# Performance work log

Measured on AMD Instinct MI355X. Metric: run time of the kernel, lower is better.

Reference implementation:

```python
import jax, jax.numpy as jnp
import numpy as np

H = 128  # hidden_size
EPS = 1e-5


def _lstm_scan(pre, Whh, h0, c0):
    # pre: [L, B, 4H] = x @ Wih^T + bias, precomputed outside the scan
    def step(carry, g_in):
        h, c = carry
        gates = g_in + h @ Whh.T  # [B, 4H], PyTorch gate order i,f,g,o
        i, f, g, o = jnp.split(gates, 4, axis=-1)
        c = jax.nn.sigmoid(f) * c + jax.nn.sigmoid(i) * jnp.tanh(g)
        h = jax.nn.sigmoid(o) * jnp.tanh(c)
        return (h, c), h
    (_, _), hs = jax.lax.scan(step, (h0, c0), pre)
    return hs  # [L, B, H]


def setup_inputs() -> dict:
    key = jax.random.key(0)
    ks = jax.random.split(key, 12)
    B, L, D = 128, 512, 256
    s = 0.05
    inp = {
        "x": jax.random.normal(ks[0], (B, L, D), jnp.float32),
        "W_proj": jax.random.normal(ks[1], (D, D), jnp.float32) * s,
        "b_proj": jnp.zeros((D,), jnp.float32),
        "Wih_f": jax.random.normal(ks[2], (4 * H, D), jnp.float32) * s,
        "Whh_f": jax.random.normal(ks[3], (4 * H, H), jnp.float32) * s,
        "b_f": jnp.concatenate([jnp.zeros(H), jnp.ones(H), jnp.zeros(2 * H)]).astype(jnp.float32),
        "Wih_b": jax.random.normal(ks[4], (4 * H, D), jnp.float32) * s,
        "Whh_b": jax.random.normal(ks[5], (4 * H, H), jnp.float32) * s,
        "b_b": jnp.concatenate([jnp.zeros(H), jnp.ones(H), jnp.zeros(2 * H)]).astype(jnp.float32),
        "gamma": jnp.ones((2 * H,), jnp.float32),
        "beta": jnp.zeros((2 * H,), jnp.float32),
    }
    return inp


def reference(x, W_proj, b_proj, Wih_f, Whh_f, b_f, Wih_b, Whh_b, b_b, gamma, beta):
    B, L, D = x.shape
    # input projection
    xp = x @ W_proj.T + b_proj  # [B, L, D]
    xt = jnp.transpose(xp, (1, 0, 2))  # time-major [L, B, D]

    h0 = jnp.zeros((B, H), x.dtype)
    c0 = jnp.zeros((B, H), x.dtype)

    # precompute input contributions to gates (big batched GEMM)
    pre_f = jnp.einsum('lbd,gd->lbg', xt, Wih_f) + b_f  # [L, B, 4H]
    pre_b = jnp.einsum('lbd,gd->lbg', xt[::-1], Wih_b) + b_b

    hs_f = _lstm_scan(pre_f, Whh_f, h0, c0)           # [L, B, H]
    hs_b = _lstm_scan(pre_b, Whh_b, h0, c0)[::-1]     # reverse back to forward time

    out = jnp.concatenate([hs_f, hs_b], axis=-1)       # [L, B, 2H]
    out = jnp.transpose(out, (1, 0, 2))                # [B, L, 2H]

    # LayerNorm over last dim (eval mode; dropout is identity)
    mu = out.mean(axis=-1, keepdims=True)
    var = out.var(axis=-1, keepdims=True)
    out = (out - mu) * jax.lax.rsqrt(var + EPS) * gamma + beta
    return out
```

## Files before the change

### kernel.cpp

```cpp
#include <hip/hip_runtime.h>

#define NB 128
#define NL 512
#define ND 256
#define NG 1024

typedef __attribute__((ext_vector_type(8))) short bfv8;
typedef __attribute__((ext_vector_type(4))) float f32x4;

#define LOG2E 1.4426950408889634f
#define NSCALE (-1.4426950408889634f)
#define GSCALE (2.8853900817779268f)

__device__ __forceinline__ unsigned short f2bf(float f) {
    unsigned u = __float_as_uint(f);
    u += 0x7fffu + ((u >> 16) & 1u);
    return (unsigned short)(u >> 16);
}
__device__ __forceinline__ float bf2f(unsigned short u) {
    return __uint_as_float(((unsigned)u) << 16);
}

__global__ __launch_bounds__(256) void convert_kernel(const float* __restrict__ x,
                                                      unsigned short* __restrict__ xbt) {
    size_t t = (size_t)blockIdx.x * 256 + threadIdx.x;
    size_t e = t * 4;
    int d = (int)(e & 255u);
    int l = (int)((e >> 8) & 511u);
    int b = (int)(e >> 17);
    float4 v = *(const float4*)(x + e);
    ushort4 o;
    o.x = f2bf(v.x); o.y = f2bf(v.y); o.z = f2bf(v.z); o.w = f2bf(v.w);
    *(ushort4*)(xbt + ((size_t)(l * NB + b)) * ND + d) = o;
}

__global__ __launch_bounds__(256) void fold_kernel(const float* __restrict__ Wproj,
                                                   const float* __restrict__ bproj,
                                                   const float* __restrict__ Wih_f,
                                                   const float* __restrict__ b_f,
                                                   const float* __restrict__ Wih_b,
                                                   const float* __restrict__ b_b,
                                                   unsigned short* __restrict__ weff,
                                                   float* __restrict__ beff) {
    int g = blockIdx.x;
    int k = threadIdx.x;
    int dirg = g >> 9;
    int rem  = g & 511;
    int hidg = rem >> 2;
    int gate = rem & 3;
    int srcrow = gate * 128 + hidg;
    float scale = (gate == 2) ? GSCALE : NSCALE;
    const float* Wih = dirg ? (Wih_b + (size_t)srcrow * ND) : (Wih_f + (size_t)srcrow * ND);
    float acc = 0.f;
    for (int d = 0; d < ND; ++d)
        acc += Wih[d] * Wproj[(size_t)d * ND + k];
    weff[(size_t)g * ND + k] = f2bf(acc * scale);
    if (k == 0) {
        float ab = dirg ? b_b[srcrow] : b_f[srcrow];
        for (int d = 0; d < ND; ++d) ab += Wih[d] * bproj[d];
        beff[g] = ab * scale;
    }
}

__global__ __launch_bounds__(256, 2) void gemm_pre(const unsigned short* __restrict__ A,
                                                   const unsigned short* __restrict__ Bw,
                                                   const float* __restrict__ bias,
                                                   unsigned short* __restrict__ C) {
    __shared__ unsigned short As[128 * 32];
    __shared__ unsigned short Bs[128 * 32];
    const int tid = threadIdx.x;
    const int lane = tid & 63;
    const int wid = tid >> 6;
    const int m0 = blockIdx.y * 128;
    const int n0 = blockIdx.x * 128;
    const int wm = (wid >> 1) * 64;
    const int wn = (wid & 1) * 64;

    f32x4 acc[4][4] = {};

    const int row0 = tid >> 2;
    const int row1 = row0 + 64;
    const int co = (tid & 3) * 8;
    const int sw = (((tid & 3) << 4) ^ ((row0 & 3) << 4)) >> 1;

    bfv8 ra0 = *(const bfv8*)(A + (size_t)(m0 + row0) * ND + co);
    bfv8 ra1 = *(const bfv8*)(A + (size_t)(m0 + row1) * ND + co);
    bfv8 rb0 = *(const bfv8*)(Bw + (size_t)(n0 + row0) * ND + co);
    bfv8 rb1 = *(const bfv8*)(Bw + (size_t)(n0 + row1) * ND + co);

    for (int it = 0; it < 8; ++it) {
        __syncthreads();
        *(bfv8*)(As + row0 * 32 + sw) = ra0;
        *(bfv8*)(As + row1 * 32 + sw) = ra1;
        *(bfv8*)(Bs + row0 * 32 + sw) = rb0;
        *(bfv8*)(Bs + row1 * 32 + sw) = rb1;
        const int k1 = ((it + 1) & 7) * 32;
        ra0 = *(const bfv8*)(A + (size_t)(m0 + row0) * ND + k1 + co);
        ra1 = *(const bfv8*)(A + (size_t)(m0 + row1) * ND + k1 + co);
        rb0 = *(const bfv8*)(Bw + (size_t)(n0 + row0) * ND + k1 + co);
        rb1 = *(const bfv8*)(Bw + (size_t)(n0 + row1) * ND + k1 + co);
        __syncthreads();

        const int r = lane & 15;
        const int kq = lane >> 4;
        bfv8 af[4], bfr[4];
        #pragma unroll
        for (int m = 0; m < 4; ++m) {
            int rw = wm + m * 16 + r;
            af[m] = *(const bfv8*)(As + rw * 32 + (((kq << 4) ^ ((rw & 3) << 4)) >> 1));
        }
        #pragma unroll
        for (int n = 0; n < 4; ++n) {
            int rw = wn + n * 16 + r;
            bfr[n] = *(const bfv8*)(Bs + rw * 32 + (((kq << 4) ^ ((rw & 3) << 4)) >> 1));
        }
        #pragma unroll
        for (int m = 0; m < 4; ++m)
            #pragma unroll
            for (int n = 0; n < 4; ++n)
                acc[m][n] = __builtin_amdgcn_mfma_f32_16x16x32_bf16(af[m], bfr[n], acc[m][n], 0, 0, 0);
    }

    const int r = lane & 15;
    const int rq = lane >> 4;
    #pragma unroll
    for (int n = 0; n < 4; ++n) {
        int col = n0 + wn + n * 16 + r;
        float bv = bias[col];
        #pragma unroll
        for (int m = 0; m < 4; ++m) {
            #pragma unroll
            for (int v = 0; v < 4; ++v) {
                int rowg = m0 + wm + m * 16 + rq * 4 + v;
                C[(size_t)rowg * NG + col] = f2bf(acc[m][n][v] + bv);
            }
        }
    }
}

struct ScanSM {
    unsigned short h[2][136];
    char pin[81700];
};

#define MFMA16(a, b, c) __builtin_amdgcn_mfma_f32_16x16x32_bf16((a), (b), (c), 0, 0, 0)

#define STEP(S, CURB, NXTB)                                                    \
  {                                                                            \
    int rr = (S) + 2; if (rr > 511) rr = 511;                \
    int tts = dirs ? (511 - rr) : rr;                                          \
    const unsigned short* rowp = pdb + (size_t)tts * (NB * NG);                \
    uint2 nx = *(const uint2*)(rowp + hid4);                \
    bfv8 ha0 = *(const bfv8*)&sm.h[CURB][q * 8];                               \
    bfv8 ha1 = *(const bfv8*)&sm.h[CURB][32 + q * 8];                          \
    bfv8 ha2 = *(const bfv8*)&sm.h[CURB][64 + q * 8];                          \
    bfv8 ha3 = *(const bfv8*)&sm.h[CURB][96 + q * 8];                          \
    f32x4 z = {0.f, 0.f, 0.f, 0.f};                                            \
    f32x4 acci = MFMA16(ha0, bfr[0][0], z);                                    \
    f32x4 accf = MFMA16(ha0, bfr[1][0], z);                                    \
    f32x4 accg = MFMA16(ha0, bfr[2][0], z);                                    \
    f32x4 acco = MFMA16(ha0, bfr[3][0], z);                                    \
    acci = MFMA16(ha1, bfr[0][1], acci); accf = MFMA16(ha1, bfr[1][1], accf);  \
    accg = MFMA16(ha1, bfr[2][1], accg); acco = MFMA16(ha1, bfr[3][1], acco);  \
    acci = MFMA16(ha2, bfr[0][2], acci); accf = MFMA16(ha2, bfr[1][2], accf);  \
    accg = MFMA16(ha2, bfr[2][2], accg); acco = MFMA16(ha2, bfr[3][2], acco);  \
    acci = MFMA16(ha3, bfr[0][3], acci); accf = MFMA16(ha3, bfr[1][3], accf);  \
    accg = MFMA16(ha3, bfr[2][3], accg); acco = MFMA16(ha3, bfr[3][3], acco);  \
    int tt = dirs ? (511 - (S)) : (S);                                         \
    {                                                                          \
        float pi = __uint_as_float(pP0.x << 16);                               \
        float pf = __uint_as_float(pP0.x & 0xffff0000u);                       \
        float pg = __uint_as_float(pP0.y << 16);                               \
        float po = __uint_as_float(pP0.y & 0xffff0000u);                       \
                 \
        float ia = __builtin_amdgcn_rcpf(1.f + __builtin_amdgcn_exp2f(acci[0] + pi)); \
        float fa = __builtin_amdgcn_rcpf(1.f + __builtin_amdgcn_exp2f(accf[0] + pf)); \
        float rg = __builtin_amdgcn_rcpf(1.f + __builtin_amdgcn_exp2f(accg[0] + pg)); \
        float oa = __builtin_amdgcn_rcpf(1.f + __builtin_amdgcn_exp2f(acco[0] + po)); \
        float ga = fmaf(-2.f, rg, 1.f);                                        \
        c0 = fmaf(fa, c0, ia * ga);                                            \
        float rc = __builtin_amdgcn_rcpf(1.f + __builtin_amdgcn_exp2f(c0 * GSCALE)); \
        float th = fmaf(-2.f, rc, 1.f);                                        \
        float hv = oa * th;                                                    \
        if (q == 0) {                                                          \
            sm.h[NXTB][hid] = f2bf(hv);                                        \
            orowb[(size_t)tt * 256 + hid] = hv;                                \
        }                                                                      \
    }                                                                          \
    pP0 = pP1; pP1 = nx;                                                       \
    __builtin_amdgcn_sched_barrier(0);                                         \
    asm volatile("s_waitcnt lgkmcnt(0)");                                      \
    __builtin_amdgcn_s_barrier();                                              \
    __builtin_amdgcn_sched_barrier(0);                                         \
  }

__global__ void __launch_bounds__(512)
scan_kernel(const unsigned short* __restrict__ pre,
            const float* __restrict__ Whh_f,
            const float* __restrict__ Whh_b,
            float* __restrict__ out) {
    const int b    = blockIdx.x;
    const int dirs = blockIdx.y;
    const int tid  = threadIdx.x;
    const int w    = tid >> 6;
    const int lane = tid & 63;
    const int r    = lane & 15;
    const int q    = lane >> 4;
    const int hid  = 16 * w + r;
    const int hid4 = hid * 4;

    __shared__ ScanSM sm;

    const float* __restrict__ Wd = dirs ? Whh_b : Whh_f;
    bfv8 bfr[4][4];
    #pragma unroll
    for (int g = 0; g < 4; ++g) {
        const float wscale = (g == 2) ? GSCALE : NSCALE;
        #pragma unroll
        for (int kk = 0; kk < 4; ++kk) {
            const float* src = Wd + (size_t)(g * 128 + hid) * 128 + kk * 32 + q * 8;
            float4 lo = *(const float4*)(src);
            float4 hi = *(const float4*)(src + 4);
            bfv8 v;
            v[0] = (short)f2bf(lo.x * wscale); v[1] = (short)f2bf(lo.y * wscale);
            v[2] = (short)f2bf(lo.z * wscale); v[3] = (short)f2bf(lo.w * wscale);
            v[4] = (short)f2bf(hi.x * wscale); v[5] = (short)f2bf(hi.y * wscale);
            v[6] = (short)f2bf(hi.z * wscale); v[7] = (short)f2bf(hi.w * wscale);
            bfr[g][kk] = v;
        }
    }

    if (q == 0) sm.h[0][hid] = 0;

    float c0 = 0.f;

    const unsigned short* pdb = pre + (size_t)b * NG + dirs * 512;
    float* orowb = out + (size_t)b * NL * 256 + dirs * 128;

    int t0 = dirs ? 511 : 0;
    int t1 = dirs ? 510 : 1;
    uint2 pP0 = *(const uint2*)(pdb + (size_t)t0 * (NB * NG) + hid4);
    uint2 pP1 = *(const uint2*)(pdb + (size_t)t1 * (NB * NG) + hid4);
    __syncthreads();

    for (int s = 0; s < 512; s += 2) {
        STEP(s, 0, 1)
        STEP(s + 1, 1, 0)
    }
}

__global__ __launch_bounds__(256) void ln_kernel(float* __restrict__ out,
                                                 const float* __restrict__ gamma,
                                                 const float* __restrict__ beta) {
    int row = blockIdx.x * 4 + (threadIdx.x >> 6);
    int lane = threadIdx.x & 63;
    float* p = out + (size_t)row * 256;
    float4 v = ((const float4*)p)[lane];
    float s = (v.x + v.y) + (v.z + v.w);
    float s2 = (v.x * v.x + v.y * v.y) + (v.z * v.z + v.w * v.w);
    #pragma unroll
    for (int o = 32; o > 0; o >>= 1) {
        s += __shfl_xor(s, o);
        s2 += __shfl_xor(s2, o);
    }
    float mu = s * (1.f / 256.f);
    float var = s2 * (1.f / 256.f) - mu * mu;
    float rs = rsqrtf(var + 1e-5f);
    float4 gv = ((const float4*)gamma)[lane];
    float4 bv = ((const float4*)beta)[lane];
    float4 r;
    r.x = (v.x - mu) * rs * gv.x + bv.x;
    r.y = (v.y - mu) * rs * gv.y + bv.y;
    r.z = (v.z - mu) * rs * gv.z + bv.z;
    r.w = (v.w - mu) * rs * gv.w + bv.w;
    ((float4*)p)[lane] = r;
}

extern "C" void kernel_launch(void* const* d_in, const int* in_sizes, int n_in,
                              void* d_out, int out_size, void* d_ws, size_t ws_size,
                              hipStream_t stream) {
    (void)in_sizes; (void)n_in; (void)out_size; (void)ws_size;
    const float* x     = (const float*)d_in[0];
    const float* Wproj = (const float*)d_in[1];
    const float* bproj = (const float*)d_in[2];
    const float* Wih_f = (const float*)d_in[3];
    const float* Whh_f = (const float*)d_in[4];
    const float* b_f   = (const float*)d_in[5];
    const float* Wih_b = (const float*)d_in[6];
    const float* Whh_b = (const float*)d_in[7];
    const float* b_b   = (const float*)d_in[8];
    const float* gamma = (const float*)d_in[9];
    const float* beta  = (const float*)d_in[10];
    float* out = (float*)d_out;

    char* ws = (char*)d_ws;
    unsigned short* pre  = (unsigned short*)ws;
    unsigned short* xbt  = (unsigned short*)(ws + 134217728);
    unsigned short* weff = (unsigned short*)(ws + 167772160);
    float*          beff = (float*)(ws + 168296448);

    convert_kernel<<<16384, 256, 0, stream>>>(x, xbt);
    fold_kernel<<<1024, 256, 0, stream>>>(Wproj, bproj, Wih_f, b_f, Wih_b, b_b, weff, beff);
    gemm_pre<<<dim3(8, 512), 256, 0, stream>>>(xbt, weff, beff, pre);
    scan_kernel<<<dim3(128, 2), 512, 0, stream>>>(pre, Whh_f, Whh_b, out);
    ln_kernel<<<16384, 256, 0, stream>>>(out, gamma, beta);
}
```

Measured before the change: 358.1 us.

## Halve scan block to 4 waves with two hidden groups; store h as bf16

The scan kernel now runs 256 threads per block instead of 512. Each wave owns two groups of 16 hidden units, doubling its MFMA work and the weight fragments it keeps in registers. Fewer waves should make the per-step block barrier cheaper, and two independent activation chains give more instruction-level parallelism. The hidden states are now written as bf16 into a reused workspace buffer and read back by the LayerNorm kernel. This halves the intermediate traffic but lowers the precision of the values LayerNorm sees.

Result: slower. 423.1 us (+18.1%).

```diff
diff --git a/kernel.cpp b/kernel.cpp
--- a/kernel.cpp
+++ b/kernel.cpp
@@ -145,60 +145,75 @@
 
 #define MFMA16(a, b, c) __builtin_amdgcn_mfma_f32_16x16x32_bf16((a), (b), (c), 0, 0, 0)
 
+#define ACT2(AI, AF, AG, AO, PP, CC, HID, NXTB)                                \
+    {                                                                          \
+        float pi = __uint_as_float(PP.x << 16);                                \
+        float pf = __uint_as_float(PP.x & 0xffff0000u);                        \
+        float pg = __uint_as_float(PP.y << 16);                                \
+        float po = __uint_as_float(PP.y & 0xffff0000u);                        \
+        float ia = __builtin_amdgcn_rcpf(1.f + __builtin_amdgcn_exp2f(AI[0] + pi)); \
+        float fa = __builtin_amdgcn_rcpf(1.f + __builtin_amdgcn_exp2f(AF[0] + pf)); \
+        float rg = __builtin_amdgcn_rcpf(1.f + __builtin_amdgcn_exp2f(AG[0] + pg)); \
+        float oa = __builtin_amdgcn_rcpf(1.f + __builtin_amdgcn_exp2f(AO[0] + po)); \
+        float ga = fmaf(-2.f, rg, 1.f);                                        \
+        CC = fmaf(fa, CC, ia * ga);                                            \
+        float rc = __builtin_amdgcn_rcpf(1.f + __builtin_amdgcn_exp2f(CC * GSCALE)); \
+        float th = fmaf(-2.f, rc, 1.f);                                        \
+        unsigned short us = f2bf(oa * th);                                     \
+        if (q == 0) {                                                          \
+            sm.h[NXTB][HID] = us;                                              \
+            hsrow[(size_t)tt * 256 + HID] = us;                                \
+        }                                                                      \
+    }
+
 #define STEP(S, CURB, NXTB)                                                    \
   {                                                                            \
     int rr = (S) + 2; if (rr > 511) rr = 511;                \
     int tts = dirs ? (511 - rr) : rr;                                          \
     const unsigned short* rowp = pdb + (size_t)tts * (NB * NG);                \
-    uint2 nx = *(const uint2*)(rowp + hid4);                \
+    uint2 nxa = *(const uint2*)(rowp + hid4a);              \
+    uint2 nxb = *(const uint2*)(rowp + hid4b);                                 \
     bfv8 ha0 = *(const bfv8*)&sm.h[CURB][q * 8];                               \
     bfv8 ha1 = *(const bfv8*)&sm.h[CURB][32 + q * 8];                          \
     bfv8 ha2 = *(const bfv8*)&sm.h[CURB][64 + q * 8];                          \
     bfv8 ha3 = *(const bfv8*)&sm.h[CURB][96 + q * 8];                          \
     f32x4 z = {0.f, 0.f, 0.f, 0.f};                                            \
-    f32x4 acci = MFMA16(ha0, bfr[0][0], z);                                    \
-    f32x4 accf = MFMA16(ha0, bfr[1][0], z);                                    \
-    f32x4 accg = MFMA16(ha0, bfr[2][0], z);                                    \
-    f32x4 acco = MFMA16(ha0, bfr[3][0], z);                                    \
-    acci = MFMA16(ha1, bfr[0][1], acci); accf = MFMA16(ha1, bfr[1][1], accf);  \
-    accg = MFMA16(ha1, bfr[2][1], accg); acco = MFMA16(ha1, bfr[3][1], acco);  \
-    acci = MFMA16(ha2, bfr[0][2], acci); accf = MFMA16(ha2, bfr[1][2], accf);  \
-    accg = MFMA16(ha2, bfr[2][2], accg); acco = MFMA16(ha2, bfr[3][2], acco);  \
-    acci = MFMA16(ha3, bfr[0][3], acci); accf = MFMA16(ha3, bfr[1][3], accf);  \
-    accg = MFMA16(ha3, bfr[2][3], accg); acco = MFMA16(ha3, bfr[3][3], acco);  \
+    f32x4 aA0 = MFMA16(ha0, bfr[0][0], z);                                     \
+    f32x4 aA1 = MFMA16(ha0, bfr[1][0], z);                                     \
+    f32x4 aA2 = MFMA16(ha0, bfr[2][0], z);                                     \
+    f32x4 aA3 = MFMA16(ha0, bfr[3][0], z);                                     \
+    f32x4 aB0 = MFMA16(ha0, bfr[4][0], z);                                     \
+    f32x4 aB1 = MFMA16(ha0, bfr[5][0], z);                                     \
+    f32x4 aB2 = MFMA16(ha0, bfr[6][0], z);                                     \
+    f32x4 aB3 = MFMA16(ha0, bfr[7][0], z);                                     \
+    aA0 = MFMA16(ha1, bfr[0][1], aA0); aA1 = MFMA16(ha1, bfr[1][1], aA1);      \
+    aA2 = MFMA16(ha1, bfr[2][1], aA2); aA3 = MFMA16(ha1, bfr[3][1], aA3);      \
+    aB0 = MFMA16(ha1, bfr[4][1], aB0); aB1 = MFMA16(ha1, bfr[5][1], aB1);      \
+    aB2 = MFMA16(ha1, bfr[6][1], aB2); aB3 = MFMA16(ha1, bfr[7][1], aB3);      \
+    aA0 = MFMA16(ha2, bfr[0][2], aA0); aA1 = MFMA16(ha2, bfr[1][2], aA1);      \
+    aA2 = MFMA16(ha2, bfr[2][2], aA2); aA3 = MFMA16(ha2, bfr[3][2], aA3);      \
+    aB0 = MFMA16(ha2, bfr[4][2], aB0); aB1 = MFMA16(ha2, bfr[5][2], aB1);      \
+    aB2 = MFMA16(ha2, bfr[6][2], aB2); aB3 = MFMA16(ha2, bfr[7][2], aB3);      \
+    aA0 = MFMA16(ha3, bfr[0][3], aA0); aA1 = MFMA16(ha3, bfr[1][3], aA1);      \
+    aA2 = MFMA16(ha3, bfr[2][3], aA2); aA3 = MFMA16(ha3, bfr[3][3], aA3);      \
+    aB0 = MFMA16(ha3, bfr[4][3], aB0); aB1 = MFMA16(ha3, bfr[5][3], aB1);      \
+    aB2 = MFMA16(ha3, bfr[6][3], aB2); aB3 = MFMA16(ha3, bfr[7][3], aB3);      \
     int tt = dirs ? (511 - (S)) : (S);                                         \
-    {                                                                          \
-        float pi = __uint_as_float(pP0.x << 16);                               \
-        float pf = __uint_as_float(pP0.x & 0xffff0000u);                       \
-        float pg = __uint_as_float(pP0.y << 16);                               \
-        float po = __uint_as_float(pP0.y & 0xffff0000u);                       \
-                 \
-        float ia = __builtin_amdgcn_rcpf(1.f + __builtin_amdgcn_exp2f(acci[0] + pi)); \
-        float fa = __builtin_amdgcn_rcpf(1.f + __builtin_amdgcn_exp2f(accf[0] + pf)); \
-        float rg = __builtin_amdgcn_rcpf(1.f + __builtin_amdgcn_exp2f(accg[0] + pg)); \
-        float oa = __builtin_amdgcn_rcpf(1.f + __builtin_amdgcn_exp2f(acco[0] + po)); \
-        float ga = fmaf(-2.f, rg, 1.f);                                        \
-        c0 = fmaf(fa, c0, ia * ga);                                            \
-        float rc = __builtin_amdgcn_rcpf(1.f + __builtin_amdgcn_exp2f(c0 * GSCALE)); \
-        float th = fmaf(-2.f, rc, 1.f);                                        \
-        float hv = oa * th;                                                    \
-        if (q == 0) {                                                          \
-            sm.h[NXTB][hid] = f2bf(hv);                                        \
-            orowb[(size_t)tt * 256 + hid] = hv;                                \
-        }                                                                      \
-    }                                                                          \
-    pP0 = pP1; pP1 = nx;                                                       \
+    ACT2(aA0, aA1, aA2, aA3, pPa0, c0a, hidA, NXTB)                            \
+    ACT2(aB0, aB1, aB2, aB3, pPb0, c0b, hidB, NXTB)                            \
+    pPa0 = pPa1; pPa1 = nxa;                                                   \
+    pPb0 = pPb1; pPb1 = nxb;                                                   \
     __builtin_amdgcn_sched_barrier(0);                                         \
     asm volatile("s_waitcnt lgkmcnt(0)");                                      \
     __builtin_amdgcn_s_barrier();                                              \
     __builtin_amdgcn_sched_barrier(0);                                         \
   }
 
-__global__ void __launch_bounds__(512)
+__global__ void __launch_bounds__(256)
 scan_kernel(const unsigned short* __restrict__ pre,
             const float* __restrict__ Whh_f,
             const float* __restrict__ Whh_b,
-            float* __restrict__ out) {
+            unsigned short* __restrict__ hs) {
     const int b    = blockIdx.x;
     const int dirs = blockIdx.y;
     const int tid  = threadIdx.x;
@@ -206,41 +221,49 @@
     const int lane = tid & 63;
     const int r    = lane & 15;
     const int q    = lane >> 4;
-    const int hid  = 16 * w + r;
-    const int hid4 = hid * 4;
+    const int hidA = 16 * w + r;
+    const int hidB = hidA + 64;
+    const int hid4a = hidA * 4;
+    const int hid4b = hidB * 4;
 
     __shared__ ScanSM sm;
 
     const float* __restrict__ Wd = dirs ? Whh_b : Whh_f;
-    bfv8 bfr[4][4];
+    bfv8 bfr[8][4];
     #pragma unroll
-    for (int g = 0; g < 4; ++g) {
-        const float wscale = (g == 2) ? GSCALE : NSCALE;
-        #pragma unroll
-        for (int kk = 0; kk < 4; ++kk) {
-            const float* src = Wd + (size_t)(g * 128 + hid) * 128 + kk * 32 + q * 8;
-            float4 lo = *(const float4*)(src);
-            float4 hi = *(const float4*)(src + 4);
-            bfv8 v;
-            v[0] = (short)f2bf(lo.x * wscale); v[1] = (short)f2bf(lo.y * wscale);
-            v[2] = (short)f2bf(lo.z * wscale); v[3] = (short)f2bf(lo.w * wscale);
-            v[4] = (short)f2bf(hi.x * wscale); v[5] = (short)f2bf(hi.y * wscale);
-            v[6] = (short)f2bf(hi.z * wscale); v[7] = (short)f2bf(hi.w * wscale);
-            bfr[g][kk] = v;
+    for (int hg = 0; hg < 2; ++hg) {
+        const int hh = 16 * w + 64 * hg + r;
+        #pragma unroll
+        for (int g = 0; g < 4; ++g) {
+            const float wscale = (g == 2) ? GSCALE : NSCALE;
+            #pragma unroll
+            for (int kk = 0; kk < 4; ++kk) {
+                const float* src = Wd + (size_t)(g * 128 + hh) * 128 + kk * 32 + q * 8;
+                float4 lo = *(const float4*)(src);
+                float4 hi = *(const float4*)(src + 4);
+                bfv8 v;
+                v[0] = (short)f2bf(lo.x * wscale); v[1] = (short)f2bf(lo.y * wscale);
+                v[2] = (short)f2bf(lo.z * wscale); v[3] = (short)f2bf(lo.w * wscale);
+                v[4] = (short)f2bf(hi.x * wscale); v[5] = (short)f2bf(hi.y * wscale);
+                v[6] = (short)f2bf(hi.z * wscale); v[7] = (short)f2bf(hi.w * wscale);
+                bfr[hg * 4 + g][kk] = v;
+            }
         }
     }
 
-    if (q == 0) sm.h[0][hid] = 0;
-
-    float c0 = 0.f;
+    if (q == 0) { sm.h[0][hidA] = 0; sm.h[0][hidB] = 0; }
+
+    float c0a = 0.f, c0b = 0.f;
 
     const unsigned short* pdb = pre + (size_t)b * NG + dirs * 512;
-    float* orowb = out + (size_t)b * NL * 256 + dirs * 128;
+    unsigned short* hsrow = hs + (size_t)b * NL * 256 + dirs * 128;
 
     int t0 = dirs ? 511 : 0;
     int t1 = dirs ? 510 : 1;
-    uint2 pP0 = *(const uint2*)(pdb + (size_t)t0 * (NB * NG) + hid4);
-    uint2 pP1 = *(const uint2*)(pdb + (size_t)t1 * (NB * NG) + hid4);
+    uint2 pPa0 = *(const uint2*)(pdb + (size_t)t0 * (NB * NG) + hid4a);
+    uint2 pPb0 = *(const uint2*)(pdb + (size_t)t0 * (NB * NG) + hid4b);
+    uint2 pPa1 = *(const uint2*)(pdb + (size_t)t1 * (NB * NG) + hid4a);
+    uint2 pPb1 = *(const uint2*)(pdb + (size_t)t1 * (NB * NG) + hid4b);
     __syncthreads();
 
     for (int s = 0; s < 512; s += 2) {
@@ -249,15 +272,16 @@
     }
 }
 
-__global__ __launch_bounds__(256) void ln_kernel(float* __restrict__ out,
+__global__ __launch_bounds__(256) void ln_kernel(const unsigned short* __restrict__ hs,
+                                                 float* __restrict__ out,
                                                  const float* __restrict__ gamma,
                                                  const float* __restrict__ beta) {
     int row = blockIdx.x * 4 + (threadIdx.x >> 6);
     int lane = threadIdx.x & 63;
-    float* p = out + (size_t)row * 256;
-    float4 v = ((const float4*)p)[lane];
-    float s = (v.x + v.y) + (v.z + v.w);
-    float s2 = (v.x * v.x + v.y * v.y) + (v.z * v.z + v.w * v.w);
+    const ushort4 hv = ((const ushort4*)(hs + (size_t)row * 256))[lane];
+    float a = bf2f(hv.x), bb = bf2f(hv.y), c = bf2f(hv.z), d = bf2f(hv.w);
+    float s = (a + bb) + (c + d);
+    float s2 = (a * a + bb * bb) + (c * c + d * d);
     #pragma unroll
     for (int o = 32; o > 0; o >>= 1) {
         s += __shfl_xor(s, o);
@@ -268,12 +292,12 @@
     float rs = rsqrtf(var + 1e-5f);
     float4 gv = ((const float4*)gamma)[lane];
     float4 bv = ((const float4*)beta)[lane];
-    float4 r;
-    r.x = (v.x - mu) * rs * gv.x + bv.x;
-    r.y = (v.y - mu) * rs * gv.y + bv.y;
-    r.z = (v.z - mu) * rs * gv.z + bv.z;
-    r.w = (v.w - mu) * rs * gv.w + bv.w;
-    ((float4*)p)[lane] = r;
+    float4 rr;
+    rr.x = (a - mu) * rs * gv.x + bv.x;
+    rr.y = (bb - mu) * rs * gv.y + bv.y;
+    rr.z = (c - mu) * rs * gv.z + bv.z;
+    rr.w = (d - mu) * rs * gv.w + bv.w;
+    ((float4*)(out + (size_t)row * 256))[lane] = rr;
 }
 
 extern "C" void kernel_launch(void* const* d_in, const int* in_sizes, int n_in,
@@ -296,12 +320,13 @@
     char* ws = (char*)d_ws;
     unsigned short* pre  = (unsigned short*)ws;
     unsigned short* xbt  = (unsigned short*)(ws + 134217728);
+    unsigned short* hs   = xbt;
     unsigned short* weff = (unsigned short*)(ws + 167772160);
     float*          beff = (float*)(ws + 168296448);
 
     convert_kernel<<<16384, 256, 0, stream>>>(x, xbt);
     fold_kernel<<<1024, 256, 0, stream>>>(Wproj, bproj, Wih_f, b_f, Wih_b, b_b, weff, beff);
     gemm_pre<<<dim3(8, 512), 256, 0, stream>>>(xbt, weff, beff, pre);
-    scan_kernel<<<dim3(128, 2), 512, 0, stream>>>(pre, Whh_f, Whh_b, out);
-    ln_kernel<<<16384, 256, 0, stream>>>(out, gamma, beta);
-}
+    scan_kernel<<<dim3(128, 2), 256, 0, stream>>>(pre, Whh_f, Whh_b, hs);
+    ln_kernel<<<16384, 256, 0, stream>>>(hs, out, gamma, beta);
+}
```
